# Performance work log

Measured on AMD Instinct MI355X. Metric: run time of the kernel, lower is better.

## Reference

```python
import jax, jax.numpy as jnp
import numpy as np

B, T, N, H, NHEADS, DFF, DEMO = 128, 128, 76, 64, 4, 256, 12

def _lin(x, W, b):
    # torch Linear: y = x @ W.T + b, W is [out, in]
    return jnp.matmul(x, W.T) + b

def _layernorm(x, g, b, eps=1e-7):
    mu = x.mean(-1, keepdims=True)
    var = ((x - mu) ** 2).mean(-1, keepdims=True)
    return (x - mu) / jnp.sqrt(var + eps) * g + b

def _gru_all_features(X, Wih, Whh, bih, bhh):
    # X: [B,T,N]; Wih: [N,3H] (input_size=1); Whh: [N,3H,H]; biases [N,3H]
    # PyTorch gate order: r, z, n. Returns H_seq [B,N,T,H].
    Bsz, Tlen, Nf = X.shape
    Hd = Whh.shape[-1]
    h0 = jnp.zeros((Bsz, Nf, Hd), X.dtype)
    def step(h, x_t):  # h [B,N,H], x_t [B,N]
        ih = x_t[:, :, None] * Wih[None] + bih[None]            # [B,N,3H]
        hh = jnp.einsum('bnh,ngh->bng', h, Whh) + bhh[None]     # [B,N,3H]
        r = jax.nn.sigmoid(ih[..., :Hd] + hh[..., :Hd])
        z = jax.nn.sigmoid(ih[..., Hd:2 * Hd] + hh[..., Hd:2 * Hd])
        n = jnp.tanh(ih[..., 2 * Hd:] + r * hh[..., 2 * Hd:])
        h_new = (1.0 - z) * n + z * h
        return h_new, h_new
    _, Hs = jax.lax.scan(step, h0, jnp.moveaxis(X, 1, 0))       # [T,B,N,H]
    return jnp.transpose(Hs, (1, 2, 0, 3))                      # [B,N,T,H]

def _time_attention(Hs, Wt, bt, Wx, bx, rate):
    # Hs [B,N,T,H]; Wt/Wx [N,H,H]; bt/bx [N,H]; rate [N]
    Tlen = Hs.shape[2]
    q = jnp.einsum('bnh,nkh->bnk', Hs[:, :, -1, :], Wt) + bt[None]          # [B,N,H]
    K = jnp.einsum('bnth,nkh->bntk', Hs, Wx) + bx[None, :, None, :]         # [B,N,T,H]
    dot = jnp.einsum('bnk,bntk->bnt', q, K)                                 # [B,N,T]
    tdecay = jnp.arange(1, Tlen + 1, dtype=Hs.dtype)                        # [1..T]
    ds = jax.nn.sigmoid(dot)
    denom = jax.nn.sigmoid(rate)[None, :, None] * jnp.log(2.72 + (1.0 - ds)) * tdecay
    denom = jnp.maximum(denom, 1e-6)
    e = jax.nn.relu(ds / denom)
    alpha = jax.nn.softmax(e, axis=-1)
    return jnp.einsum('bnt,bnth->bnh', alpha, Hs)                           # [B,N,H]

def _mha_decov(x, Wq, bq, Wk, bk, Wv, bv, Wo, bo, n_heads):
    Bsz, L, Dm = x.shape
    dk = Dm // n_heads
    def split(t):
        return t.reshape(Bsz, L, n_heads, dk).transpose(0, 2, 1, 3)
    q, k, v = split(_lin(x, Wq, bq)), split(_lin(x, Wk, bk)), split(_lin(x, Wv, bv))
    scores = jnp.matmul(q, k.transpose(0, 1, 3, 2)) / (dk ** 0.5)
    attn = jax.nn.softmax(scores, axis=-1)
    head = jnp.matmul(attn, v)                                              # [B,h,L,dk]
    merged = head.transpose(0, 2, 1, 3).reshape(Bsz, L, Dm)
    out = _lin(merged, Wo, bo)
    U = merged.reshape(Bsz * L, Dm)
    U = U - U.mean(0, keepdims=True)
    C = (U.T @ U) / max(Bsz * L, 1)
    decov = 0.5 * ((C ** 2).sum() - (jnp.diag(C) ** 2).sum())
    return out, decov

def setup_inputs():
    key = jax.random.key(0)
    ks = jax.random.split(key, 32)
    s = 0.08
    def rn(k, shape):
        return jax.random.normal(k, shape, jnp.float32) * s
    inp = {
        'X': jax.random.normal(ks[0], (B, T, N), jnp.float32),
        'D': jax.random.normal(ks[1], (B, DEMO), jnp.float32),
        'gru_Wih': rn(ks[2], (N, 3 * H)),
        'gru_Whh': rn(ks[3], (N, 3 * H, H)),
        'gru_bih': jnp.zeros((N, 3 * H), jnp.float32),
        'gru_bhh': jnp.zeros((N, 3 * H), jnp.float32),
        'att_Wt': rn(ks[4], (N, H, H)),
        'att_bt': jnp.zeros((N, H), jnp.float32),
        'att_Wx': rn(ks[5], (N, H, H)),
        'att_bx': jnp.zeros((N, H), jnp.float32),
        'att_rate': jnp.zeros((N,), jnp.float32),
        'demo_W': rn(ks[6], (H, DEMO)),
        'demo_b': jnp.zeros((H,), jnp.float32),
        'mh_Wq': rn(ks[7], (H, H)), 'mh_bq': rn(ks[8], (H,)),
        'mh_Wk': rn(ks[9], (H, H)), 'mh_bk': rn(ks[10], (H,)),
        'mh_Wv': rn(ks[11], (H, H)), 'mh_bv': rn(ks[12], (H,)),
        'mh_Wo': rn(ks[13], (H, H)), 'mh_bo': rn(ks[14], (H,)),
        'ln1_g': jnp.ones((H,), jnp.float32), 'ln1_b': jnp.zeros((H,), jnp.float32),
        'ffn_W1': rn(ks[15], (DFF, H)), 'ffn_b1': rn(ks[16], (DFF,)),
        'ffn_W2': rn(ks[17], (H, DFF)), 'ffn_b2': rn(ks[18], (H,)),
        'ln2_g': jnp.ones((H,), jnp.float32), 'ln2_b': jnp.zeros((H,), jnp.float32),
        'fa_Wq': rn(ks[19], (H, H)), 'fa_bq': rn(ks[20], (H,)),
        'fa_Wk': rn(ks[21], (H, H)), 'fa_bk': rn(ks[22], (H,)),
        'fa_Wv': rn(ks[23], (H, H)), 'fa_bv': rn(ks[24], (H,)),
        'fa_Wout': rn(ks[25], (1, H)), 'fa_bout': rn(ks[26], (1,)),
        'out0_W': rn(ks[27], (H, H)), 'out0_b': jnp.zeros((H,), jnp.float32),
        'out1_W': rn(ks[28], (1, H)), 'out1_b': jnp.zeros((1,), jnp.float32),
    }
    return inp

def _forward(X, D, gru_Wih, gru_Whh, gru_bih, gru_bhh, att_Wt, att_bt, att_Wx, att_bx,
             att_rate, demo_W, demo_b, mh_Wq, mh_bq, mh_Wk, mh_bk, mh_Wv, mh_bv, mh_Wo,
             mh_bo, ln1_g, ln1_b, ffn_W1, ffn_b1, ffn_W2, ffn_b2, ln2_g, ln2_b,
             fa_Wq, fa_bq, fa_Wk, fa_bk, fa_Wv, fa_bv, fa_Wout, fa_bout,
             out0_W, out0_b, out1_W, out1_b):
    Hs = _gru_all_features(X, gru_Wih, gru_Whh, gru_bih, gru_bhh)   # [B,N,T,H]
    F_dyn = _time_attention(Hs, att_Wt, att_bt, att_Wx, att_bx, att_rate)  # [B,N,H]
    f_demo = jnp.tanh(_lin(D, demo_W, demo_b))[:, None, :]
    F_in = jnp.concatenate([F_dyn, f_demo], axis=1)                 # [B,N+1,H]
    _, decov = _mha_decov(F_in, mh_Wq, mh_bq, mh_Wk, mh_bk, mh_Wv, mh_bv, mh_Wo, mh_bo, NHEADS)
    attn_out, _ = _mha_decov(_layernorm(F_in, ln1_g, ln1_b), mh_Wq, mh_bq, mh_Wk, mh_bk,
                             mh_Wv, mh_bv, mh_Wo, mh_bo, NHEADS)
    Y = F_in + attn_out
    z = _layernorm(Y, ln2_g, ln2_b)
    Z = Y + _lin(jax.nn.relu(_lin(z, ffn_W1, ffn_b1)), ffn_W2, ffn_b2)
    # FinalAttentionQKV
    Q = _lin(Z, fa_Wq, fa_bq)
    K = _lin(Z, fa_Wk, fa_bk)
    V = _lin(Z, fa_Wv, fa_bv)
    scores = _lin(Q * K, fa_Wout, fa_bout)[..., 0]                  # [B,L]
    alpha = jax.nn.softmax(scores, axis=1)
    s = jnp.einsum('bl,blh->bh', alpha, V)
    h = jax.nn.relu(_lin(s, out0_W, out0_b))
    y_prob = jax.nn.sigmoid(_lin(h, out1_W, out1_b))
    return y_prob, decov

def reference(X, D, gru_Wih, gru_Whh, gru_bih, gru_bhh, att_Wt, att_bt, att_Wx, att_bx,
              att_rate, demo_W, demo_b, mh_Wq, mh_bq, mh_Wk, mh_bk, mh_Wv, mh_bv, mh_Wo,
              mh_bo, ln1_g, ln1_b, ffn_W1, ffn_b1, ffn_W2, ffn_b2, ln2_g, ln2_b,
              fa_Wq, fa_bq, fa_Wk, fa_bk, fa_Wv, fa_bv, fa_Wout, fa_bout,
              out0_W, out0_b, out1_W, out1_b):
    return _forward(X, D, gru_Wih, gru_Whh, gru_bih, gru_bhh, att_Wt, att_bt, att_Wx,
                    att_bx, att_rate, demo_W, demo_b, mh_Wq, mh_bq, mh_Wk, mh_bk, mh_Wv,
                    mh_bv, mh_Wo, mh_bo, ln1_g, ln1_b, ffn_W1, ffn_b1, ffn_W2, ffn_b2,
                    ln2_g, ln2_b, fa_Wq, fa_bq, fa_Wk, fa_bk, fa_Wv, fa_bv, fa_Wout,
                    fa_bout, out0_W, out0_b, out1_W, out1_b)
```

## Files before the change

kernel.cpp:

```cpp
#include <hip/hip_runtime.h>
#include <math.h>

#define B_ 128
#define T_ 128
#define NF 76
#define HD 64
#define LQ 77

typedef __attribute__((ext_vector_type(8))) short short8v;
typedef __attribute__((ext_vector_type(4))) short short4v;
typedef __attribute__((ext_vector_type(4))) float f32x4;

__device__ __forceinline__ float frcp(float x) { return __builtin_amdgcn_rcpf(x); }
__device__ __forceinline__ float sigmf(float x) { return frcp(1.0f + __expf(-x)); }
__device__ __forceinline__ float sigm2(float x) { return frcp(1.0f + __builtin_amdgcn_exp2f(-x)); }
__device__ __forceinline__ float tanh_fast(float x) { return 2.0f * frcp(1.0f + __expf(-2.0f * x)) - 1.0f; }
__device__ __forceinline__ short tobf(float x) {
    unsigned u = __float_as_uint(x);
    u += 0x7FFF + ((u >> 16) & 1);
    return (short)(u >> 16);
}
__device__ __forceinline__ float bflo(unsigned u) { return __uint_as_float(u << 16); }
__device__ __forceinline__ float bfhi(unsigned u) { return __uint_as_float(u & 0xffff0000u); }

__global__ __launch_bounds__(256) void k_gru0(
    const float* __restrict__ X, const float* __restrict__ Wih,
    const float* __restrict__ Whh, const float* __restrict__ bih,
    const float* __restrict__ bhh,
    const float* __restrict__ Wt, const float* __restrict__ bt,
    const float* __restrict__ Wx, const float* __restrict__ bx,
    short* __restrict__ Hsg, float* __restrict__ qxg, float* __restrict__ qbg)
{
    __shared__ short As[8][16 * 68];
    __shared__ float xs[16 * 129];
    __shared__ float q1[16 * 65];
    __shared__ float q2[16 * 65];

    const int nf = blockIdx.y;
    const int chunk = blockIdx.x;
    const int cbase = chunk * 16;
    const int tid = threadIdx.x;
    const int w = tid >> 6;
    const int lane = tid & 63;
    const int col = lane & 15;
    const int quad = lane >> 4;

    const float S1 = 1.44269504f;
    const float S2 = 2.88539008f;

    for (int i = tid; i < 16 * T_; i += 256) {
        int b = i >> 7, t = i & 127;
        xs[b * 129 + t] = X[((size_t)(cbase + b) * T_ + t) * NF + nf];
    }

    short8v bfr[3][2];
    const float* wbase = Whh + (size_t)nf * 12288;
#pragma unroll
    for (int g3 = 0; g3 < 3; ++g3) {
        const float sc = (g3 == 2) ? S2 : S1;
#pragma unroll
        for (int k2 = 0; k2 < 2; ++k2) {
            int g = 64 * g3 + 16 * w + col;
            const float* src = wbase + g * 64 + 32 * k2 + quad * 8;
            float4 f0 = *(const float4*)src;
            float4 f1 = *(const float4*)(src + 4);
            short8v fr;
            fr[0] = tobf(f0.x * sc); fr[1] = tobf(f0.y * sc);
            fr[2] = tobf(f0.z * sc); fr[3] = tobf(f0.w * sc);
            fr[4] = tobf(f1.x * sc); fr[5] = tobf(f1.y * sc);
            fr[6] = tobf(f1.z * sc); fr[7] = tobf(f1.w * sc);
            bfr[g3][k2] = fr;
        }
    }

    const int c = 16 * w + col;
    const int base = nf * 192;
    const float wr = Wih[base + c] * S1;
    const float wz = Wih[base + 64 + c] * S1;
    const float wn = Wih[base + 128 + c] * S2;
    const float br = (bih[base + c] + bhh[base + c]) * S1;
    const float bz = (bih[base + 64 + c] + bhh[base + 64 + c]) * S1;
    const float bnn = bih[base + 128 + c] * S2;
    const float bhn = bhh[base + 128 + c] * S2;

    for (int i = tid; i < 16 * 68; i += 256) As[7][i] = 0;
    float hold[4];
#pragma unroll
    for (int r = 0; r < 4; ++r) hold[r] = 0.0f;
    __syncthreads();

    for (int t = 0; t < T_; ++t) {
        const int rb = (t + 7) & 7;
        const int wb = t & 7;
        const short* ap = &As[rb][col * 68 + quad * 8];
        short4v a0 = *(const short4v*)ap;
        short4v a1 = *(const short4v*)(ap + 4);
        short4v a2 = *(const short4v*)(ap + 32);
        short4v a3 = *(const short4v*)(ap + 36);
        short8v A0 = {a0[0], a0[1], a0[2], a0[3], a1[0], a1[1], a1[2], a1[3]};
        short8v A1 = {a2[0], a2[1], a2[2], a2[3], a3[0], a3[1], a3[2], a3[3]};

        f32x4 acc[3];
#pragma unroll
        for (int g3 = 0; g3 < 3; ++g3) {
            f32x4 a = {0.0f, 0.0f, 0.0f, 0.0f};
            a = __builtin_amdgcn_mfma_f32_16x16x32_bf16(A0, bfr[g3][0], a, 0, 0, 0);
            a = __builtin_amdgcn_mfma_f32_16x16x32_bf16(A1, bfr[g3][1], a, 0, 0, 0);
            acc[g3] = a;
        }

#pragma unroll
        for (int r = 0; r < 4; ++r) {
            float xv = xs[(quad * 4 + r) * 129 + t];
            float rr = sigm2(xv * wr + br + acc[0][r]);
            float zz = sigm2(xv * wz + bz + acc[1][r]);
            float nn = 2.0f * sigm2(xv * wn + bnn + rr * (acc[2][r] + bhn)) - 1.0f;
            hold[r] = nn + zz * (hold[r] - nn);
        }

#pragma unroll
        for (int r = 0; r < 4; ++r)
            As[wb][(quad * 4 + r) * 68 + c] = tobf(hold[r]);
        __syncthreads();

        if ((t & 7) == 7) {
            const int oct = tid & 7, bb = (tid >> 3) & 15, k0 = tid >> 7;
            short4v r0[4], r1[4];
#pragma unroll
            for (int s = 0; s < 4; ++s) {
                const short* p = &As[k0 + 2 * s][bb * 68 + oct * 8];
                r0[s] = *(const short4v*)p;
                r1[s] = *(const short4v*)(p + 4);
            }
            __syncthreads();
            const size_t gbase =
                (((size_t)nf * 128 + cbase + bb) * 128 + (t - 7)) * 64 + oct * 8;
#pragma unroll
            for (int s = 0; s < 4; ++s) {
                short8v v = {r0[s][0], r0[s][1], r0[s][2], r0[s][3],
                             r1[s][0], r1[s][1], r1[s][2], r1[s][3]};
                *(short8v*)(Hsg + gbase + (size_t)(k0 + 2 * s) * 64) = v;
            }
        }
    }

#pragma unroll
    for (int r = 0; r < 4; ++r)
        q1[(quad * 4 + r) * 65 + c] = hold[r];
    __syncthreads();
    for (int o = tid; o < 16 * 64; o += 256) {
        int b = o >> 6, k = o & 63;
        const float* wrow = Wt + ((size_t)nf * 64 + k) * 64;
        float a = bt[nf * 64 + k];
#pragma unroll 8
        for (int h = 0; h < 64; h += 4) {
            float4 wv = *(const float4*)&wrow[h];
            a += q1[b * 65 + h] * wv.x + q1[b * 65 + h + 1] * wv.y
               + q1[b * 65 + h + 2] * wv.z + q1[b * 65 + h + 3] * wv.w;
        }
        q2[b * 65 + k] = a;
    }
    __syncthreads();
    for (int o = tid; o < 16 * 64; o += 256) {
        int b = o >> 6, h = o & 63;
        float a = 0.0f;
#pragma unroll 8
        for (int k = 0; k < 64; ++k)
            a += q2[b * 65 + k] * Wx[((size_t)nf * 64 + k) * 64 + h];
        qxg[((size_t)nf * 128 + cbase + b) * 64 + h] = a;
    }
    for (int b = tid; b < 16; b += 256) {
        float a = 0.0f;
        for (int k = 0; k < 64; ++k) a += q2[b * 65 + k] * bx[nf * 64 + k];
        qbg[nf * 128 + cbase + b] = a;
    }
}

__global__ __launch_bounds__(128) void k_att(
    const short* __restrict__ Hsg, const float* __restrict__ qxg,
    const float* __restrict__ qbg, const float* __restrict__ rate,
    const float* __restrict__ D, const float* __restrict__ dW,
    const float* __restrict__ db, float* __restrict__ Sz,
    float* __restrict__ Fin)
{
    const int nf = blockIdx.x, b = blockIdx.y;
    const int tid = threadIdx.x;

    if (nf == NF) {
        if (tid < 64) {
            float acc = db[tid];
            for (int j = 0; j < 12; ++j) acc += D[b * 12 + j] * dW[tid * 12 + j];
            Fin[((size_t)b * LQ + 76) * HD + tid] = tanh_fast(acc);
        }
        int s0 = b * 33;
        for (int k = tid; k < 33; k += 128) {
            int idx = s0 + k;
            if (idx < 4161) Sz[idx] = 0.0f;
        }
        return;
    }

    __shared__ float wsum[128 * 69];
    __shared__ float wl[128];
    __shared__ float qxl[64];
    __shared__ float pn[2][68];
    __shared__ float pd[2];
    if (tid < 64) qxl[tid] = qxg[((size_t)nf * 128 + b) * 64 + tid];
    const float qb = qbg[nf * 128 + b];
    const float sigr = sigmf(rate[nf]);

    uint4 rv[8];
    const uint4* src = (const uint4*)(Hsg + (((size_t)nf * 128 + b) * 128 + tid) * 64);
#pragma unroll
    for (int k = 0; k < 8; ++k) rv[k] = src[k];
    __syncthreads();

    float a = qb;
#pragma unroll
    for (int k = 0; k < 8; ++k) {
        a += bflo(rv[k].x) * qxl[k * 8 + 0] + bfhi(rv[k].x) * qxl[k * 8 + 1]
           + bflo(rv[k].y) * qxl[k * 8 + 2] + bfhi(rv[k].y) * qxl[k * 8 + 3]
           + bflo(rv[k].z) * qxl[k * 8 + 4] + bfhi(rv[k].z) * qxl[k * 8 + 5]
           + bflo(rv[k].w) * qxl[k * 8 + 6] + bfhi(rv[k].w) * qxl[k * 8 + 7];
    }
    float ds = sigmf(a);
    float dn = fmaxf(sigr * __logf(2.72f + (1.0f - ds)) * (float)(tid + 1), 1e-6f);
    float e = fmaxf(ds * frcp(dn), 0.0f);
    float w = __expf(e);
    wl[tid] = w;
#pragma unroll
    for (int k = 0; k < 8; ++k) {
        float* d = &wsum[tid * 69 + k * 8];
        d[0] = w * bflo(rv[k].x); d[1] = w * bfhi(rv[k].x);
        d[2] = w * bflo(rv[k].y); d[3] = w * bfhi(rv[k].y);
        d[4] = w * bflo(rv[k].z); d[5] = w * bfhi(rv[k].z);
        d[6] = w * bflo(rv[k].w); d[7] = w * bfhi(rv[k].w);
    }
    __syncthreads();
    {
        int ch = tid & 63, half = tid >> 6;
        float acc = 0.0f, den = 0.0f;
        int t0 = half * 64;
        for (int t = t0; t < t0 + 64; ++t) {
            acc += wsum[t * 69 + ch];
            den += wl[t];
        }
        pn[half][ch] = acc;
        if (ch == 0) pd[half] = den;
    }
    __syncthreads();
    if (tid < 64) {
        float num = pn[0][tid] + pn[1][tid];
        float den = pd[0] + pd[1];
        Fin[((size_t)b * LQ + nf) * HD + tid] = num * frcp(den);
    }
}

// ... 529 lines not shown
                int b = o >> 6, h = o & 63;
                float a = 0.0f;
#pragma unroll 8
                for (int k = 0; k < 64; ++k)
                    a += q2[b * 65 + k] * Wx[((size_t)nf * 64 + k) * 64 + h];
                q1[b * 65 + h] = a;
            }
            for (int b = tid; b < 16; b += 128) {
                float a = 0.0f;
                for (int k = 0; k < 64; ++k) a += q2[b * 65 + k] * bx[nf * 64 + k];
                qbs[b] = a;
            }
            __syncthreads();
#pragma unroll
            for (int r = 0; r < 4; ++r) {
                qbv[r] = qbs[quad * 4 + r];
#pragma unroll
                for (int s = 0; s < 2; ++s)
                    qxv[s][r] = q1[(quad * 4 + r) * 65 + 32 * w + 16 * s + col];
                den[r] = 0.0f; num[0][r] = 0.0f; num[1][r] = 0.0f;
            }
            __syncthreads();
        }
    }
#pragma unroll
    for (int s = 0; s < 2; ++s)
#pragma unroll
        for (int r = 0; r < 4; ++r) {
            int b = cbase + quad * 4 + r;
            int c = 32 * w + 16 * s + col;
            Fin[((size_t)b * LQ + nf) * HD + c] = num[s][r] * frcp(den[r]);
        }
}

extern "C" void kernel_launch(void* const* d_in, const int* in_sizes, int n_in,
                              void* d_out, int out_size, void* d_ws, size_t ws_size,
                              hipStream_t stream)
{
    (void)in_sizes; (void)n_in; (void)out_size;
    const float* X     = (const float*)d_in[0];
    const float* D     = (const float*)d_in[1];
    const float* gWih  = (const float*)d_in[2];
    const float* gWhh  = (const float*)d_in[3];
    const float* gbih  = (const float*)d_in[4];
    const float* gbhh  = (const float*)d_in[5];
    const float* aWt   = (const float*)d_in[6];
    const float* abt   = (const float*)d_in[7];
    const float* aWx   = (const float*)d_in[8];
    const float* abx   = (const float*)d_in[9];
    const float* arate = (const float*)d_in[10];
    const float* dW    = (const float*)d_in[11];
    const float* db    = (const float*)d_in[12];
    const float* mWq   = (const float*)d_in[13]; const float* mbq = (const float*)d_in[14];
    const float* mWk   = (const float*)d_in[15]; const float* mbk = (const float*)d_in[16];
    const float* mWv   = (const float*)d_in[17]; const float* mbv = (const float*)d_in[18];
    const float* mWo   = (const float*)d_in[19]; const float* mbo = (const float*)d_in[20];
    const float* l1g   = (const float*)d_in[21]; const float* l1b = (const float*)d_in[22];
    const float* fW1   = (const float*)d_in[23]; const float* fb1 = (const float*)d_in[24];
    const float* fW2   = (const float*)d_in[25]; const float* fb2 = (const float*)d_in[26];
    const float* l2g   = (const float*)d_in[27]; const float* l2b = (const float*)d_in[28];
    const float* faWq  = (const float*)d_in[29]; const float* fabq = (const float*)d_in[30];
    const float* faWk  = (const float*)d_in[31]; const float* fabk = (const float*)d_in[32];
    const float* faWv  = (const float*)d_in[33]; const float* fabv = (const float*)d_in[34];
    const float* faWo  = (const float*)d_in[35]; const float* fabo = (const float*)d_in[36];
    const float* o0W   = (const float*)d_in[37]; const float* o0b  = (const float*)d_in[38];
    const float* o1W   = (const float*)d_in[39]; const float* o1b  = (const float*)d_in[40];

    float* ws  = (float*)d_ws;
    float* Fin = ws;
    float* M1  = Fin + 630784;
    float* M2  = M1  + 630784;
    float* S   = M2  + 630784;
    float* MU  = S   + 4096;
    unsigned* cnt = (unsigned*)(MU + 64);
    float* qxg = MU + 128;
    float* scout = qxg + 622592;
    short* Hsg = (short*)(scout + 9856);
    const size_t need = (size_t)(630784 * 3 + 4096 + 128 + 622592 + 9856) * 4
                        + (size_t)79691776 * 2;
    float* outp = (float*)d_out;
    float* qbg = scout;

    if (ws_size >= need) {
        k_gru0<<<dim3(8, NF), 256, 0, stream>>>(X, gWih, gWhh, gbih, gbhh,
                                                aWt, abt, aWx, abx, Hsg, qxg, qbg);
        k_att<<<dim3(NF + 1, B_), 128, 0, stream>>>(Hsg, qxg, qbg, arate,
                                                    D, dW, db, S, Fin);
    } else {
        k_gru_mfma<<<dim3(8, NF), 128, 0, stream>>>(X, gWih, gWhh, gbih, gbhh,
                                                    aWt, abt, aWx, abx, arate, Fin);
        k_demo<<<B_, 64, 0, stream>>>(D, dW, db, Fin);
        k_zero<<<1, 256, 0, stream>>>(S);
    }
    k_mha2<<<dim3(B_, 4, 2), 256, 0, stream>>>(Fin, mWq, mbq, mWk, mbk, mWv, mbv,
                                               l1g, l1b, M1, M2);
    k_zff<<<616, 256, 0, stream>>>(Fin, M2, mWo, mbo, l2g, l2b,
                                   fW1, fb1, fW2, fb2,
                                   faWq, fabq, faWk, fabk, faWv, fabv,
                                   faWo, fabo, scout);
    k_cov<<<dim3(16, 32), 256, 0, stream>>>(M1, S, MU, cnt, outp);
    k_head<<<B_, 128, 0, stream>>>(M2, scout, o0W, o0b, o1W, o1b, outp);
}
```

Before: 519.6 us.

## Process two GRU features per block to interleave independent recurrences

Each GRU block now handles two adjacent features, so two independent recurrent chains share one time-step loop and barrier, which lets MFMA and transcendental latency of one chain overlap the other. Gate biases are folded into the MFMA accumulator init, the x loads become float2, and s_setprio is raised around the MFMA section. The grid halves to 8x38 blocks, so fewer waves are resident across the device, and register use per thread roughly doubles for the weight fragments.

```diff
diff --git a/kernel.cpp b/kernel.cpp
--- a/kernel.cpp
+++ b/kernel.cpp
@@ -31,14 +31,13 @@
     const float* __restrict__ Wx, const float* __restrict__ bx,
     short* __restrict__ Hsg, float* __restrict__ qxg, float* __restrict__ qbg)
 {
-    __shared__ short As[8][16 * 68];
-    __shared__ float xs[16 * 129];
+    __shared__ short As[2][8][16 * 68];
+    __shared__ float2 xs2[16 * 129];
     __shared__ float q1[16 * 65];
     __shared__ float q2[16 * 65];
 
-    const int nf = blockIdx.y;
-    const int chunk = blockIdx.x;
-    const int cbase = chunk * 16;
+    const int nf0 = blockIdx.y * 2;
+    const int cbase = blockIdx.x * 16;
     const int tid = threadIdx.x;
     const int w = tid >> 6;
     const int lane = tid & 63;
@@ -50,129 +49,167 @@
 
     for (int i = tid; i < 16 * T_; i += 256) {
         int b = i >> 7, t = i & 127;
-        xs[b * 129 + t] = X[((size_t)(cbase + b) * T_ + t) * NF + nf];
-    }
-
-    short8v bfr[3][2];
-    const float* wbase = Whh + (size_t)nf * 12288;
-#pragma unroll
-    for (int g3 = 0; g3 < 3; ++g3) {
-        const float sc = (g3 == 2) ? S2 : S1;
-#pragma unroll
-        for (int k2 = 0; k2 < 2; ++k2) {
-            int g = 64 * g3 + 16 * w + col;
-            const float* src = wbase + g * 64 + 32 * k2 + quad * 8;
-            float4 f0 = *(const float4*)src;
-            float4 f1 = *(const float4*)(src + 4);
-            short8v fr;
-            fr[0] = tobf(f0.x * sc); fr[1] = tobf(f0.y * sc);
-            fr[2] = tobf(f0.z * sc); fr[3] = tobf(f0.w * sc);
-            fr[4] = tobf(f1.x * sc); fr[5] = tobf(f1.y * sc);
-            fr[6] = tobf(f1.z * sc); fr[7] = tobf(f1.w * sc);
-            bfr[g3][k2] = fr;
-        }
+        xs2[b * 129 + t] = *(const float2*)&X[((size_t)(cbase + b) * T_ + t) * NF + nf0];
     }
 
     const int c = 16 * w + col;
-    const int base = nf * 192;
-    const float wr = Wih[base + c] * S1;
-    const float wz = Wih[base + 64 + c] * S1;
-    const float wn = Wih[base + 128 + c] * S2;
-    const float br = (bih[base + c] + bhh[base + c]) * S1;
-    const float bz = (bih[base + 64 + c] + bhh[base + 64 + c]) * S1;
-    const float bnn = bih[base + 128 + c] * S2;
-    const float bhn = bhh[base + 128 + c] * S2;
-
-    for (int i = tid; i < 16 * 68; i += 256) As[7][i] = 0;
-    float hold[4];
-#pragma unroll
-    for (int r = 0; r < 4; ++r) hold[r] = 0.0f;
+
+    short8v bfr[2][3][2];
+    f32x4 biasC[2][3];
+    float wrv[2], wzv[2], wnv[2], bnnv[2];
+#pragma unroll
+    for (int f = 0; f < 2; ++f) {
+        const float* wbase = Whh + (size_t)(nf0 + f) * 12288;
+#pragma unroll
+        for (int g3 = 0; g3 < 3; ++g3) {
+            const float sc = (g3 == 2) ? S2 : S1;
+#pragma unroll
+            for (int k2 = 0; k2 < 2; ++k2) {
+                int g = 64 * g3 + 16 * w + col;
+                const float* src = wbase + g * 64 + 32 * k2 + quad * 8;
+                float4 f0 = *(const float4*)src;
+                float4 f1 = *(const float4*)(src + 4);
+                short8v fr;
+                fr[0] = tobf(f0.x * sc); fr[1] = tobf(f0.y * sc);
+                fr[2] = tobf(f0.z * sc); fr[3] = tobf(f0.w * sc);
+                fr[4] = tobf(f1.x * sc); fr[5] = tobf(f1.y * sc);
+                fr[6] = tobf(f1.z * sc); fr[7] = tobf(f1.w * sc);
+                bfr[f][g3][k2] = fr;
+            }
+        }
+        const int base = (nf0 + f) * 192;
+        wrv[f] = Wih[base + c] * S1;
+        wzv[f] = Wih[base + 64 + c] * S1;
+        wnv[f] = Wih[base + 128 + c] * S2;
+        bnnv[f] = bih[base + 128 + c] * S2;
+        float brr = (bih[base + c] + bhh[base + c]) * S1;
+        float bzz = (bih[base + 64 + c] + bhh[base + 64 + c]) * S1;
+        float bhn = bhh[base + 128 + c] * S2;
+        biasC[f][0] = (f32x4){brr, brr, brr, brr};
+        biasC[f][1] = (f32x4){bzz, bzz, bzz, bzz};
+        biasC[f][2] = (f32x4){bhn, bhn, bhn, bhn};
+    }
+
+    {
+        short* Ap = &As[0][0][0];
+        for (int i = tid; i < 1088; i += 256) {
+            Ap[7 * 1088 + i] = 0;
+            Ap[15 * 1088 + i] = 0;
+        }
+    }
+    float hold[2][4];
+#pragma unroll
+    for (int f = 0; f < 2; ++f)
+#pragma unroll
+        for (int r = 0; r < 4; ++r) hold[f][r] = 0.0f;
     __syncthreads();
 
     for (int t = 0; t < T_; ++t) {
         const int rb = (t + 7) & 7;
         const int wb = t & 7;
-        const short* ap = &As[rb][col * 68 + quad * 8];
-        short4v a0 = *(const short4v*)ap;
-        short4v a1 = *(const short4v*)(ap + 4);
-        short4v a2 = *(const short4v*)(ap + 32);
-        short4v a3 = *(const short4v*)(ap + 36);
-        short8v A0 = {a0[0], a0[1], a0[2], a0[3], a1[0], a1[1], a1[2], a1[3]};
-        short8v A1 = {a2[0], a2[1], a2[2], a2[3], a3[0], a3[1], a3[2], a3[3]};
-
-        f32x4 acc[3];
-#pragma unroll
-        for (int g3 = 0; g3 < 3; ++g3) {
-            f32x4 a = {0.0f, 0.0f, 0.0f, 0.0f};
-            a = __builtin_amdgcn_mfma_f32_16x16x32_bf16(A0, bfr[g3][0], a, 0, 0, 0);
-            a = __builtin_amdgcn_mfma_f32_16x16x32_bf16(A1, bfr[g3][1], a, 0, 0, 0);
-            acc[g3] = a;
-        }
+
+        short8v A0[2], A1[2];
+#pragma unroll
+        for (int f = 0; f < 2; ++f) {
+            const short* ap = &As[f][rb][col * 68 + quad * 8];
+            short4v a0 = *(const short4v*)ap;
+            short4v a1 = *(const short4v*)(ap + 4);
+            short4v a2 = *(const short4v*)(ap + 32);
+            short4v a3 = *(const short4v*)(ap + 36);
+            A0[f] = (short8v){a0[0], a0[1], a0[2], a0[3], a1[0], a1[1], a1[2], a1[3]};
+            A1[f] = (short8v){a2[0], a2[1], a2[2], a2[3], a3[0], a3[1], a3[2], a3[3]};
+        }
+
+        __builtin_amdgcn_s_setprio(1);
+        f32x4 acc[2][3];
+#pragma unroll
+        for (int f = 0; f < 2; ++f)
+#pragma unroll
+            for (int g3 = 0; g3 < 3; ++g3) {
+                f32x4 a = __builtin_amdgcn_mfma_f32_16x16x32_bf16(
+                    A0[f], bfr[f][g3][0], biasC[f][g3], 0, 0, 0);
+                acc[f][g3] = __builtin_amdgcn_mfma_f32_16x16x32_bf16(
+                    A1[f], bfr[f][g3][1], a, 0, 0, 0);
+            }
+        __builtin_amdgcn_s_setprio(0);
 
 #pragma unroll
         for (int r = 0; r < 4; ++r) {
-            float xv = xs[(quad * 4 + r) * 129 + t];
-            float rr = sigm2(xv * wr + br + acc[0][r]);
-            float zz = sigm2(xv * wz + bz + acc[1][r]);
-            float nn = 2.0f * sigm2(xv * wn + bnn + rr * (acc[2][r] + bhn)) - 1.0f;
-            hold[r] = nn + zz * (hold[r] - nn);
-        }
-
-#pragma unroll
-        for (int r = 0; r < 4; ++r)
-            As[wb][(quad * 4 + r) * 68 + c] = tobf(hold[r]);
+            float2 xv2 = xs2[(quad * 4 + r) * 129 + t];
+            float xvf[2] = {xv2.x, xv2.y};
+#pragma unroll
+            for (int f = 0; f < 2; ++f) {
+                float xv = xvf[f];
+                float rr = sigm2(fmaf(xv, wrv[f], acc[f][0][r]));
+                float zz = sigm2(fmaf(xv, wzv[f], acc[f][1][r]));
+                float uu = sigm2(fmaf(rr, acc[f][2][r], fmaf(xv, wnv[f], bnnv[f])));
+                float nn = fmaf(2.0f, uu, -1.0f);
+                hold[f][r] = fmaf(zz, hold[f][r] - nn, nn);
+                As[f][wb][(quad * 4 + r) * 68 + c] = tobf(hold[f][r]);
+            }
+        }
         __syncthreads();
 
         if ((t & 7) == 7) {
             const int oct = tid & 7, bb = (tid >> 3) & 15, k0 = tid >> 7;
-            short4v r0[4], r1[4];
-#pragma unroll
-            for (int s = 0; s < 4; ++s) {
-                const short* p = &As[k0 + 2 * s][bb * 68 + oct * 8];
-                r0[s] = *(const short4v*)p;
-                r1[s] = *(const short4v*)(p + 4);
-            }
+            short4v r0[2][4], r1[2][4];
+#pragma unroll
+            for (int f = 0; f < 2; ++f)
+#pragma unroll
+                for (int s = 0; s < 4; ++s) {
+                    const short* p = &As[f][k0 + 2 * s][bb * 68 + oct * 8];
+                    r0[f][s] = *(const short4v*)p;
+                    r1[f][s] = *(const short4v*)(p + 4);
+                }
             __syncthreads();
-            const size_t gbase =
-                (((size_t)nf * 128 + cbase + bb) * 128 + (t - 7)) * 64 + oct * 8;
-#pragma unroll
-            for (int s = 0; s < 4; ++s) {
-                short8v v = {r0[s][0], r0[s][1], r0[s][2], r0[s][3],
-                             r1[s][0], r1[s][1], r1[s][2], r1[s][3]};
-                *(short8v*)(Hsg + gbase + (size_t)(k0 + 2 * s) * 64) = v;
-            }
-        }
-    }
-
-#pragma unroll
-    for (int r = 0; r < 4; ++r)
-        q1[(quad * 4 + r) * 65 + c] = hold[r];
-    __syncthreads();
-    for (int o = tid; o < 16 * 64; o += 256) {
-        int b = o >> 6, k = o & 63;
-        const float* wrow = Wt + ((size_t)nf * 64 + k) * 64;
-        float a = bt[nf * 64 + k];
+#pragma unroll
+            for (int f = 0; f < 2; ++f) {
+                const size_t gbase =
+                    (((size_t)(nf0 + f) * 128 + cbase + bb) * 128 + (t - 7)) * 64 + oct * 8;
+#pragma unroll
+                for (int s = 0; s < 4; ++s) {
+                    short8v v = {r0[f][s][0], r0[f][s][1], r0[f][s][2], r0[f][s][3],
+                                 r1[f][s][0], r1[f][s][1], r1[f][s][2], r1[f][s][3]};
+                    *(short8v*)(Hsg + gbase + (size_t)(k0 + 2 * s) * 64) = v;
+                }
+            }
+        }
+    }
+
+#pragma unroll
+    for (int f = 0; f < 2; ++f) {
+        const int nf = nf0 + f;
+        __syncthreads();
+#pragma unroll
+        for (int r = 0; r < 4; ++r)
+            q1[(quad * 4 + r) * 65 + c] = hold[f][r];
+        __syncthreads();
+        for (int o = tid; o < 16 * 64; o += 256) {
+            int b = o >> 6, k = o & 63;
+            const float* wrow = Wt + ((size_t)nf * 64 + k) * 64;
+            float a = bt[nf * 64 + k];
 #pragma unroll 8
-        for (int h = 0; h < 64; h += 4) {
-            float4 wv = *(const float4*)&wrow[h];
-            a += q1[b * 65 + h] * wv.x + q1[b * 65 + h + 1] * wv.y
-               + q1[b * 65 + h + 2] * wv.z + q1[b * 65 + h + 3] * wv.w;
-        }
-        q2[b * 65 + k] = a;
-    }
-    __syncthreads();
-    for (int o = tid; o < 16 * 64; o += 256) {
-        int b = o >> 6, h = o & 63;
-        float a = 0.0f;
+            for (int h = 0; h < 64; h += 4) {
+                float4 wv = *(const float4*)&wrow[h];
+                a += q1[b * 65 + h] * wv.x + q1[b * 65 + h + 1] * wv.y
+                   + q1[b * 65 + h + 2] * wv.z + q1[b * 65 + h + 3] * wv.w;
+            }
+            q2[b * 65 + k] = a;
+        }
+        __syncthreads();
+        for (int o = tid; o < 16 * 64; o += 256) {
+            int b = o >> 6, h = o & 63;
+            float a = 0.0f;
 #pragma unroll 8
-        for (int k = 0; k < 64; ++k)
-            a += q2[b * 65 + k] * Wx[((size_t)nf * 64 + k) * 64 + h];
-        qxg[((size_t)nf * 128 + cbase + b) * 64 + h] = a;
-    }
-    for (int b = tid; b < 16; b += 256) {
-        float a = 0.0f;
-        for (int k = 0; k < 64; ++k) a += q2[b * 65 + k] * bx[nf * 64 + k];
-        qbg[nf * 128 + cbase + b] = a;
+            for (int k = 0; k < 64; ++k)
+                a += q2[b * 65 + k] * Wx[((size_t)nf * 64 + k) * 64 + h];
+            qxg[((size_t)nf * 128 + cbase + b) * 64 + h] = a;
+        }
+        for (int b = tid; b < 16; b += 256) {
+            float a = 0.0f;
+            for (int k = 0; k < 64; ++k) a += q2[b * 65 + k] * bx[nf * 64 + k];
+            qbg[nf * 128 + cbase + b] = a;
+        }
     }
 }
 
@@ -868,7 +905,7 @@
     float* qbg = scout;
 
     if (ws_size >= need) {
-        k_gru0<<<dim3(8, NF), 256, 0, stream>>>(X, gWih, gWhh, gbih, gbhh,
+        k_gru0<<<dim3(8, 38), 256, 0, stream>>>(X, gWih, gWhh, gbih, gbhh,
                                                 aWt, abt, aWx, abx, Hsg, qxg, qbg);
         k_att<<<dim3(NF + 1, B_), 128, 0, stream>>>(Hsg, qxg, qbg, arate,
                                                     D, dW, db, S, Fin);
```

Measured after the change: 561.7 us. 8.1% more time.

## Run each GRU recurrence block as a single wavefront to drop barriers

Applied to the files above, without the earlier changes.

The GRU kernel moves from four wavefronts per block, each owning 16 hidden columns, to one 64-lane wavefront that owns all 64 columns. Each lane now keeps 24 weight fragments in registers and issues 24 MFMAs per step. Because the whole block is one wavefront, the per-step __syncthreads and the periodic spill barriers go away, so the sequential recurrence no longer pays for cross-wave synchronisation. The time loop is unrolled by 8 with s_setprio around the MFMAs, and the epilogue projections are restructured for a single wave. The cost is much higher register pressure and four times fewer threads across the grid to hide latency.

```diff
diff --git a/kernel.cpp b/kernel.cpp
--- a/kernel.cpp
+++ b/kernel.cpp
@@ -23,7 +23,7 @@
 __device__ __forceinline__ float bflo(unsigned u) { return __uint_as_float(u << 16); }
 __device__ __forceinline__ float bfhi(unsigned u) { return __uint_as_float(u & 0xffff0000u); }
 
-__global__ __launch_bounds__(256) void k_gru0(
+__global__ __launch_bounds__(64) void k_gru0(
     const float* __restrict__ X, const float* __restrict__ Wih,
     const float* __restrict__ Whh, const float* __restrict__ bih,
     const float* __restrict__ bhh,
@@ -31,148 +31,185 @@
     const float* __restrict__ Wx, const float* __restrict__ bx,
     short* __restrict__ Hsg, float* __restrict__ qxg, float* __restrict__ qbg)
 {
-    __shared__ short As[8][16 * 68];
-    __shared__ float xs[16 * 129];
-    __shared__ float q1[16 * 65];
-    __shared__ float q2[16 * 65];
+    __shared__ short As[8 * 1088];
+    __shared__ float scratch[2176];
 
     const int nf = blockIdx.y;
-    const int chunk = blockIdx.x;
-    const int cbase = chunk * 16;
-    const int tid = threadIdx.x;
-    const int w = tid >> 6;
-    const int lane = tid & 63;
-    const int col = lane & 15;
-    const int quad = lane >> 4;
+    const int cbase = blockIdx.x * 16;
+    const int lane = threadIdx.x;
+    const int c15 = lane & 15;
+    const int q = lane >> 4;
 
     const float S1 = 1.44269504f;
     const float S2 = 2.88539008f;
 
-    for (int i = tid; i < 16 * T_; i += 256) {
+    for (int i = lane; i < 2048; i += 64) {
         int b = i >> 7, t = i & 127;
-        xs[b * 129 + t] = X[((size_t)(cbase + b) * T_ + t) * NF + nf];
-    }
-
-    short8v bfr[3][2];
+        scratch[b * 130 + t] = X[((size_t)(cbase + b) * T_ + t) * NF + nf];
+    }
+
+    short8v bfr[3][4][2];
     const float* wbase = Whh + (size_t)nf * 12288;
 #pragma unroll
     for (int g3 = 0; g3 < 3; ++g3) {
         const float sc = (g3 == 2) ? S2 : S1;
 #pragma unroll
-        for (int k2 = 0; k2 < 2; ++k2) {
-            int g = 64 * g3 + 16 * w + col;
-            const float* src = wbase + g * 64 + 32 * k2 + quad * 8;
-            float4 f0 = *(const float4*)src;
-            float4 f1 = *(const float4*)(src + 4);
-            short8v fr;
-            fr[0] = tobf(f0.x * sc); fr[1] = tobf(f0.y * sc);
-            fr[2] = tobf(f0.z * sc); fr[3] = tobf(f0.w * sc);
-            fr[4] = tobf(f1.x * sc); fr[5] = tobf(f1.y * sc);
-            fr[6] = tobf(f1.z * sc); fr[7] = tobf(f1.w * sc);
-            bfr[g3][k2] = fr;
-        }
-    }
-
-    const int c = 16 * w + col;
-    const int base = nf * 192;
-    const float wr = Wih[base + c] * S1;
-    const float wz = Wih[base + 64 + c] * S1;
-    const float wn = Wih[base + 128 + c] * S2;
-    const float br = (bih[base + c] + bhh[base + c]) * S1;
-    const float bz = (bih[base + 64 + c] + bhh[base + 64 + c]) * S1;
-    const float bnn = bih[base + 128 + c] * S2;
-    const float bhn = bhh[base + 128 + c] * S2;
-
-    for (int i = tid; i < 16 * 68; i += 256) As[7][i] = 0;
-    float hold[4];
-#pragma unroll
-    for (int r = 0; r < 4; ++r) hold[r] = 0.0f;
-    __syncthreads();
-
-    for (int t = 0; t < T_; ++t) {
-        const int rb = (t + 7) & 7;
-        const int wb = t & 7;
-        const short* ap = &As[rb][col * 68 + quad * 8];
-        short4v a0 = *(const short4v*)ap;
-        short4v a1 = *(const short4v*)(ap + 4);
-        short4v a2 = *(const short4v*)(ap + 32);
-        short4v a3 = *(const short4v*)(ap + 36);
-        short8v A0 = {a0[0], a0[1], a0[2], a0[3], a1[0], a1[1], a1[2], a1[3]};
-        short8v A1 = {a2[0], a2[1], a2[2], a2[3], a3[0], a3[1], a3[2], a3[3]};
-
-        f32x4 acc[3];
-#pragma unroll
-        for (int g3 = 0; g3 < 3; ++g3) {
-            f32x4 a = {0.0f, 0.0f, 0.0f, 0.0f};
-            a = __builtin_amdgcn_mfma_f32_16x16x32_bf16(A0, bfr[g3][0], a, 0, 0, 0);
-            a = __builtin_amdgcn_mfma_f32_16x16x32_bf16(A1, bfr[g3][1], a, 0, 0, 0);
-            acc[g3] = a;
-        }
-
-#pragma unroll
-        for (int r = 0; r < 4; ++r) {
-            float xv = xs[(quad * 4 + r) * 129 + t];
-            float rr = sigm2(xv * wr + br + acc[0][r]);
-            float zz = sigm2(xv * wz + bz + acc[1][r]);
-            float nn = 2.0f * sigm2(xv * wn + bnn + rr * (acc[2][r] + bhn)) - 1.0f;
-            hold[r] = nn + zz * (hold[r] - nn);
-        }
-
+        for (int n = 0; n < 4; ++n)
+#pragma unroll
+            for (int k2 = 0; k2 < 2; ++k2) {
+                int g = 64 * g3 + 16 * n + c15;
+                const float* src = wbase + g * 64 + 32 * k2 + q * 8;
+                float4 f0 = *(const float4*)src;
+                float4 f1 = *(const float4*)(src + 4);
+                short8v fr;
+                fr[0] = tobf(f0.x * sc); fr[1] = tobf(f0.y * sc);
+                fr[2] = tobf(f0.z * sc); fr[3] = tobf(f0.w * sc);
+                fr[4] = tobf(f1.x * sc); fr[5] = tobf(f1.y * sc);
+                fr[6] = tobf(f1.z * sc); fr[7] = tobf(f1.w * sc);
+                bfr[g3][n][k2] = fr;
+            }
+    }
+
+    float wrv[4], wzv[4], wnv[4], brv[4], bzv[4], bnnv[4], bhnv[4];
+    {
+        const int base = nf * 192;
+#pragma unroll
+        for (int n = 0; n < 4; ++n) {
+            int j = 16 * n + c15;
+            wrv[n] = Wih[base + j] * S1;
+            brv[n] = (bih[base + j] + bhh[base + j]) * S1;
+            wzv[n] = Wih[base + 64 + j] * S1;
+            bzv[n] = (bih[base + 64 + j] + bhh[base + 64 + j]) * S1;
+            wnv[n] = Wih[base + 128 + j] * S2;
+            bnnv[n] = bih[base + 128 + j] * S2;
+            bhnv[n] = bhh[base + 128 + j] * S2;
+        }
+    }
+
+    {
+        short8v z8 = {0, 0, 0, 0, 0, 0, 0, 0};
+        for (int i = lane; i < 136; i += 64)
+            *(short8v*)&As[7 * 1088 + i * 8] = z8;
+    }
+    float hold[4][4];
+#pragma unroll
+    for (int n = 0; n < 4; ++n)
+#pragma unroll
+        for (int r = 0; r < 4; ++r) hold[n][r] = 0.0f;
+
+    const f32x4 zc = {0.0f, 0.0f, 0.0f, 0.0f};
+
+    for (int tt = 0; tt < 16; ++tt) {
+#pragma unroll
+        for (int u = 0; u < 8; ++u) {
+            const int t = tt * 8 + u;
+            const int rb = (u + 7) & 7;
+            const int wb = u;
+            const short* ap = &As[rb * 1088 + c15 * 68 + q * 8];
+            short4v a0 = *(const short4v*)ap;
+            short4v a1 = *(const short4v*)(ap + 4);
+            short4v a2 = *(const short4v*)(ap + 32);
+            short4v a3 = *(const short4v*)(ap + 36);
+            short8v A0 = {a0[0], a0[1], a0[2], a0[3], a1[0], a1[1], a1[2], a1[3]};
+            short8v A1 = {a2[0], a2[1], a2[2], a2[3], a3[0], a3[1], a3[2], a3[3]};
+
+            float xv[4];
+#pragma unroll
+            for (int r = 0; r < 4; ++r)
+                xv[r] = scratch[(q * 4 + r) * 130 + t];
+
+            __builtin_amdgcn_s_setprio(1);
+            f32x4 acc[3][4];
+#pragma unroll
+            for (int g3 = 0; g3 < 3; ++g3)
+#pragma unroll
+                for (int n = 0; n < 4; ++n) {
+                    f32x4 a = __builtin_amdgcn_mfma_f32_16x16x32_bf16(
+                        A0, bfr[g3][n][0], zc, 0, 0, 0);
+                    acc[g3][n] = __builtin_amdgcn_mfma_f32_16x16x32_bf16(
+                        A1, bfr[g3][n][1], a, 0, 0, 0);
+                }
+            __builtin_amdgcn_s_setprio(0);
+
+#pragma unroll
+            for (int n = 0; n < 4; ++n)
+#pragma unroll
+                for (int r = 0; r < 4; ++r) {
+                    float rr = sigm2(fmaf(xv[r], wrv[n], brv[n]) + acc[0][n][r]);
+                    float zz = sigm2(fmaf(xv[r], wzv[n], bzv[n]) + acc[1][n][r]);
+                    float uu = sigm2(fmaf(rr, acc[2][n][r] + bhnv[n],
+                                          fmaf(xv[r], wnv[n], bnnv[n])));
+                    float nn = fmaf(2.0f, uu, -1.0f);
+                    hold[n][r] = fmaf(zz, hold[n][r] - nn, nn);
+                    As[wb * 1088 + (q * 4 + r) * 68 + 16 * n + c15] = tobf(hold[n][r]);
+                }
+        }
+        {
+            const int oct = lane & 7, b8 = lane >> 3;
+#pragma unroll
+            for (int s = 0; s < 16; ++s) {
+                int k = s >> 1, b = b8 + 8 * (s & 1);
+                const short* p = &As[k * 1088 + b * 68 + oct * 8];
+                uint2 lo = *(const uint2*)p;
+                uint2 hi = *(const uint2*)(p + 4);
+                uint4 v = {lo.x, lo.y, hi.x, hi.y};
+                *(uint4*)(Hsg + (((size_t)nf * 128 + cbase + b) * 128
+                                 + (tt * 8 + k)) * 64 + oct * 8) = v;
+            }
+        }
+    }
+
+    float* h32 = scratch;
+    float* q2s = scratch + 1088;
+#pragma unroll
+    for (int n = 0; n < 4; ++n)
 #pragma unroll
         for (int r = 0; r < 4; ++r)
-            As[wb][(quad * 4 + r) * 68 + c] = tobf(hold[r]);
-        __syncthreads();
-
-        if ((t & 7) == 7) {
-            const int oct = tid & 7, bb = (tid >> 3) & 15, k0 = tid >> 7;
-            short4v r0[4], r1[4];
-#pragma unroll
-            for (int s = 0; s < 4; ++s) {
-                const short* p = &As[k0 + 2 * s][bb * 68 + oct * 8];
-                r0[s] = *(const short4v*)p;
-                r1[s] = *(const short4v*)(p + 4);
-            }
-            __syncthreads();
-            const size_t gbase =
-                (((size_t)nf * 128 + cbase + bb) * 128 + (t - 7)) * 64 + oct * 8;
-#pragma unroll
-            for (int s = 0; s < 4; ++s) {
-                short8v v = {r0[s][0], r0[s][1], r0[s][2], r0[s][3],
-                             r1[s][0], r1[s][1], r1[s][2], r1[s][3]};
-                *(short8v*)(Hsg + gbase + (size_t)(k0 + 2 * s) * 64) = v;
-            }
-        }
-    }
-
-#pragma unroll
-    for (int r = 0; r < 4; ++r)
-        q1[(quad * 4 + r) * 65 + c] = hold[r];
-    __syncthreads();
-    for (int o = tid; o < 16 * 64; o += 256) {
-        int b = o >> 6, k = o & 63;
-        const float* wrow = Wt + ((size_t)nf * 64 + k) * 64;
-        float a = bt[nf * 64 + k];
-#pragma unroll 8
-        for (int h = 0; h < 64; h += 4) {
-            float4 wv = *(const float4*)&wrow[h];
-            a += q1[b * 65 + h] * wv.x + q1[b * 65 + h + 1] * wv.y
-               + q1[b * 65 + h + 2] * wv.z + q1[b * 65 + h + 3] * wv.w;
-        }
-        q2[b * 65 + k] = a;
-    }
-    __syncthreads();
-    for (int o = tid; o < 16 * 64; o += 256) {
-        int b = o >> 6, h = o & 63;
+            h32[(q * 4 + r) * 68 + 16 * n + c15] = hold[n][r];
+
+    {
+        const int b = lane & 15, kg = lane >> 4;
+#pragma unroll 4
+        for (int kk = 0; kk < 16; ++kk) {
+            int k = kg * 16 + kk;
+            const float4* wrow = (const float4*)(Wt + ((size_t)nf * 64 + k) * 64);
+            float a = bt[nf * 64 + k];
+#pragma unroll 4
+            for (int h4 = 0; h4 < 16; ++h4) {
+                float4 wv = wrow[h4];
+                float4 hh = *(const float4*)&h32[b * 68 + h4 * 4];
+                a += hh.x * wv.x + hh.y * wv.y + hh.z * wv.z + hh.w * wv.w;
+            }
+            q2s[b * 68 + k] = a;
+        }
+    }
+
+    {
+        float accq[16];
+#pragma unroll
+        for (int b = 0; b < 16; ++b) accq[b] = 0.0f;
+        const float* wxb = Wx + (size_t)nf * 4096 + lane;
+        for (int k4 = 0; k4 < 16; ++k4) {
+            float w0 = wxb[(k4 * 4 + 0) * 64];
+            float w1 = wxb[(k4 * 4 + 1) * 64];
+            float w2 = wxb[(k4 * 4 + 2) * 64];
+            float w3 = wxb[(k4 * 4 + 3) * 64];
+#pragma unroll
+            for (int b = 0; b < 16; ++b) {
+                float4 qv = *(const float4*)&q2s[b * 68 + k4 * 4];
+                accq[b] += qv.x * w0 + qv.y * w1 + qv.z * w2 + qv.w * w3;
+            }
+        }
+#pragma unroll
+        for (int b = 0; b < 16; ++b)
+            qxg[((size_t)nf * 128 + cbase + b) * 64 + lane] = accq[b];
+    }
+
+    if (lane < 16) {
         float a = 0.0f;
-#pragma unroll 8
         for (int k = 0; k < 64; ++k)
-            a += q2[b * 65 + k] * Wx[((size_t)nf * 64 + k) * 64 + h];
-        qxg[((size_t)nf * 128 + cbase + b) * 64 + h] = a;
-    }
-    for (int b = tid; b < 16; b += 256) {
-        float a = 0.0f;
-        for (int k = 0; k < 64; ++k) a += q2[b * 65 + k] * bx[nf * 64 + k];
-        qbg[nf * 128 + cbase + b] = a;
+            a += q2s[lane * 68 + k] * bx[nf * 64 + k];
+        qbg[nf * 128 + cbase + lane] = a;
     }
 }
 
@@ -868,8 +905,8 @@
     float* qbg = scout;
 
     if (ws_size >= need) {
-        k_gru0<<<dim3(8, NF), 256, 0, stream>>>(X, gWih, gWhh, gbih, gbhh,
-                                                aWt, abt, aWx, abx, Hsg, qxg, qbg);
+        k_gru0<<<dim3(8, NF), 64, 0, stream>>>(X, gWih, gWhh, gbih, gbhh,
+                                               aWt, abt, aWx, abx, Hsg, qxg, qbg);
         k_att<<<dim3(NF + 1, B_), 128, 0, stream>>>(Hsg, qxg, qbg, arate,
                                                     D, dW, db, S, Fin);
     } else {
```

New measurement: 573.7 us. 1.1x slower.

## Split GRU recurrence into 8-batch blocks with 2 waves each covering two column tiles

Applied to the files above, without the earlier changes.

The GRU kernel now processes 8 batch rows per block using 128 threads (2 waves), each wave handling two 16-column tiles. The grid doubles to 16x76 blocks, which gives more parallelism for the serial time loop. The batch dimension is padded to 16 inside the MFMA, so half the rows are wasted work. Biases are folded into the MFMA accumulator init, and s_setprio is wrapped around the MFMA section. Each block keeps more weight fragments in registers, and the final projection layout is adjusted to match.

```diff
diff --git a/kernel.cpp b/kernel.cpp
--- a/kernel.cpp
+++ b/kernel.cpp
@@ -23,7 +23,7 @@
 __device__ __forceinline__ float bflo(unsigned u) { return __uint_as_float(u << 16); }
 __device__ __forceinline__ float bfhi(unsigned u) { return __uint_as_float(u & 0xffff0000u); }
 
-__global__ __launch_bounds__(256) void k_gru0(
+__global__ __launch_bounds__(128) void k_gru0(
     const float* __restrict__ X, const float* __restrict__ Wih,
     const float* __restrict__ Whh, const float* __restrict__ bih,
     const float* __restrict__ bhh,
@@ -31,68 +31,73 @@
     const float* __restrict__ Wx, const float* __restrict__ bx,
     short* __restrict__ Hsg, float* __restrict__ qxg, float* __restrict__ qbg)
 {
-    __shared__ short As[8][16 * 68];
-    __shared__ float xs[16 * 129];
-    __shared__ float q1[16 * 65];
-    __shared__ float q2[16 * 65];
+    __shared__ short As[8 * 1088];
+    __shared__ float scratch[1104];
 
     const int nf = blockIdx.y;
-    const int chunk = blockIdx.x;
-    const int cbase = chunk * 16;
+    const int cbase = blockIdx.x * 8;
     const int tid = threadIdx.x;
     const int w = tid >> 6;
     const int lane = tid & 63;
-    const int col = lane & 15;
+    const int c15 = lane & 15;
     const int quad = lane >> 4;
 
     const float S1 = 1.44269504f;
     const float S2 = 2.88539008f;
 
-    for (int i = tid; i < 16 * T_; i += 256) {
+    for (int i = tid; i < 8 * 128; i += 128) {
         int b = i >> 7, t = i & 127;
-        xs[b * 129 + t] = X[((size_t)(cbase + b) * T_ + t) * NF + nf];
-    }
-
-    short8v bfr[3][2];
+        scratch[b * 130 + t] = X[((size_t)(cbase + b) * T_ + t) * NF + nf];
+    }
+
+    short8v bfr[3][2][2];
+    f32x4 biasC[3][2];
+    float wrv[2], wzv[2], wnv[2], bnnv[2];
     const float* wbase = Whh + (size_t)nf * 12288;
-#pragma unroll
-    for (int g3 = 0; g3 < 3; ++g3) {
-        const float sc = (g3 == 2) ? S2 : S1;
-#pragma unroll
-        for (int k2 = 0; k2 < 2; ++k2) {
-            int g = 64 * g3 + 16 * w + col;
-            const float* src = wbase + g * 64 + 32 * k2 + quad * 8;
-            float4 f0 = *(const float4*)src;
-            float4 f1 = *(const float4*)(src + 4);
-            short8v fr;
-            fr[0] = tobf(f0.x * sc); fr[1] = tobf(f0.y * sc);
-            fr[2] = tobf(f0.z * sc); fr[3] = tobf(f0.w * sc);
-            fr[4] = tobf(f1.x * sc); fr[5] = tobf(f1.y * sc);
-            fr[6] = tobf(f1.z * sc); fr[7] = tobf(f1.w * sc);
-            bfr[g3][k2] = fr;
-        }
-    }
-
-    const int c = 16 * w + col;
     const int base = nf * 192;
-    const float wr = Wih[base + c] * S1;
-    const float wz = Wih[base + 64 + c] * S1;
-    const float wn = Wih[base + 128 + c] * S2;
-    const float br = (bih[base + c] + bhh[base + c]) * S1;
-    const float bz = (bih[base + 64 + c] + bhh[base + 64 + c]) * S1;
-    const float bnn = bih[base + 128 + c] * S2;
-    const float bhn = bhh[base + 128 + c] * S2;
-
-    for (int i = tid; i < 16 * 68; i += 256) As[7][i] = 0;
-    float hold[4];
-#pragma unroll
-    for (int r = 0; r < 4; ++r) hold[r] = 0.0f;
+#pragma unroll
+    for (int n2 = 0; n2 < 2; ++n2) {
+        const int j = 16 * (2 * w + n2) + c15;
+#pragma unroll
+        for (int g3 = 0; g3 < 3; ++g3) {
+            const float sc = (g3 == 2) ? S2 : S1;
+#pragma unroll
+            for (int k2 = 0; k2 < 2; ++k2) {
+                const float* src = wbase + (64 * g3 + j) * 64 + 32 * k2 + quad * 8;
+                float4 f0 = *(const float4*)src;
+                float4 f1 = *(const float4*)(src + 4);
+                short8v fr;
+                fr[0] = tobf(f0.x * sc); fr[1] = tobf(f0.y * sc);
+                fr[2] = tobf(f0.z * sc); fr[3] = tobf(f0.w * sc);
+                fr[4] = tobf(f1.x * sc); fr[5] = tobf(f1.y * sc);
+                fr[6] = tobf(f1.z * sc); fr[7] = tobf(f1.w * sc);
+                bfr[g3][n2][k2] = fr;
+            }
+        }
+        wrv[n2] = Wih[base + j] * S1;
+        wzv[n2] = Wih[base + 64 + j] * S1;
+        wnv[n2] = Wih[base + 128 + j] * S2;
+        bnnv[n2] = bih[base + 128 + j] * S2;
+        float brr = (bih[base + j] + bhh[base + j]) * S1;
+        float bzz = (bih[base + 64 + j] + bhh[base + 64 + j]) * S1;
+        float bhn = bhh[base + 128 + j] * S2;
+        biasC[0][n2] = (f32x4){brr, brr, brr, brr};
+        biasC[1][n2] = (f32x4){bzz, bzz, bzz, bzz};
+        biasC[2][n2] = (f32x4){bhn, bhn, bhn, bhn};
+    }
+
+    for (int i = tid; i < 1088; i += 128) As[7 * 1088 + i] = 0;
+    float hold[2][4];
+#pragma unroll
+    for (int n2 = 0; n2 < 2; ++n2)
+#pragma unroll
+        for (int r = 0; r < 4; ++r) hold[n2][r] = 0.0f;
     __syncthreads();
 
     for (int t = 0; t < T_; ++t) {
         const int rb = (t + 7) & 7;
         const int wb = t & 7;
-        const short* ap = &As[rb][col * 68 + quad * 8];
+        const short* ap = &As[rb * 1088 + c15 * 68 + quad * 8];
         short4v a0 = *(const short4v*)ap;
         short4v a1 = *(const short4v*)(ap + 4);
         short4v a2 = *(const short4v*)(ap + 32);
@@ -100,41 +105,51 @@
         short8v A0 = {a0[0], a0[1], a0[2], a0[3], a1[0], a1[1], a1[2], a1[3]};
         short8v A1 = {a2[0], a2[1], a2[2], a2[3], a3[0], a3[1], a3[2], a3[3]};
 
-        f32x4 acc[3];
-#pragma unroll
-        for (int g3 = 0; g3 < 3; ++g3) {
-            f32x4 a = {0.0f, 0.0f, 0.0f, 0.0f};
-            a = __builtin_amdgcn_mfma_f32_16x16x32_bf16(A0, bfr[g3][0], a, 0, 0, 0);
-            a = __builtin_amdgcn_mfma_f32_16x16x32_bf16(A1, bfr[g3][1], a, 0, 0, 0);
-            acc[g3] = a;
-        }
-
-#pragma unroll
-        for (int r = 0; r < 4; ++r) {
-            float xv = xs[(quad * 4 + r) * 129 + t];
-            float rr = sigm2(xv * wr + br + acc[0][r]);
-            float zz = sigm2(xv * wz + bz + acc[1][r]);
-            float nn = 2.0f * sigm2(xv * wn + bnn + rr * (acc[2][r] + bhn)) - 1.0f;
-            hold[r] = nn + zz * (hold[r] - nn);
-        }
-
+        float xv[4];
 #pragma unroll
         for (int r = 0; r < 4; ++r)
-            As[wb][(quad * 4 + r) * 68 + c] = tobf(hold[r]);
+            xv[r] = scratch[((quad * 4 + r) & 7) * 130 + t];
+
+        __builtin_amdgcn_s_setprio(1);
+        f32x4 acc[3][2];
+#pragma unroll
+        for (int g3 = 0; g3 < 3; ++g3)
+#pragma unroll
+            for (int n2 = 0; n2 < 2; ++n2) {
+                f32x4 a = __builtin_amdgcn_mfma_f32_16x16x32_bf16(
+                    A0, bfr[g3][n2][0], biasC[g3][n2], 0, 0, 0);
+                acc[g3][n2] = __builtin_amdgcn_mfma_f32_16x16x32_bf16(
+                    A1, bfr[g3][n2][1], a, 0, 0, 0);
+            }
+        __builtin_amdgcn_s_setprio(0);
+
+#pragma unroll
+        for (int n2 = 0; n2 < 2; ++n2)
+#pragma unroll
+            for (int r = 0; r < 4; ++r) {
+                float rr = sigm2(fmaf(xv[r], wrv[n2], acc[0][n2][r]));
+                float zz = sigm2(fmaf(xv[r], wzv[n2], acc[1][n2][r]));
+                float uu = sigm2(fmaf(rr, acc[2][n2][r],
+                                      fmaf(xv[r], wnv[n2], bnnv[n2])));
+                float nn = fmaf(2.0f, uu, -1.0f);
+                hold[n2][r] = fmaf(zz, hold[n2][r] - nn, nn);
+                As[wb * 1088 + (quad * 4 + r) * 68 + 16 * (2 * w + n2) + c15]
+                    = tobf(hold[n2][r]);
+            }
         __syncthreads();
 
         if ((t & 7) == 7) {
-            const int oct = tid & 7, bb = (tid >> 3) & 15, k0 = tid >> 7;
+            const int oct = tid & 7, row = (tid >> 3) & 7, k0 = tid >> 6;
             short4v r0[4], r1[4];
 #pragma unroll
             for (int s = 0; s < 4; ++s) {
-                const short* p = &As[k0 + 2 * s][bb * 68 + oct * 8];
+                const short* p = &As[(k0 + 2 * s) * 1088 + row * 68 + oct * 8];
                 r0[s] = *(const short4v*)p;
                 r1[s] = *(const short4v*)(p + 4);
             }
             __syncthreads();
             const size_t gbase =
-                (((size_t)nf * 128 + cbase + bb) * 128 + (t - 7)) * 64 + oct * 8;
+                (((size_t)nf * 128 + cbase + row) * 128 + (t - 7)) * 64 + oct * 8;
 #pragma unroll
             for (int s = 0; s < 4; ++s) {
                 short8v v = {r0[s][0], r0[s][1], r0[s][2], r0[s][3],
@@ -144,35 +159,44 @@
         }
     }
 
-#pragma unroll
-    for (int r = 0; r < 4; ++r)
-        q1[(quad * 4 + r) * 65 + c] = hold[r];
-    __syncthreads();
-    for (int o = tid; o < 16 * 64; o += 256) {
+    __syncthreads();
+    float* h32 = scratch;
+    float* q2s = scratch + 544;
+    if (quad < 2) {
+#pragma unroll
+        for (int n2 = 0; n2 < 2; ++n2)
+#pragma unroll
+            for (int r = 0; r < 4; ++r)
+                h32[(quad * 4 + r) * 68 + 16 * (2 * w + n2) + c15] = hold[n2][r];
+    }
+    __syncthreads();
+
+    for (int o = tid; o < 512; o += 128) {
         int b = o >> 6, k = o & 63;
-        const float* wrow = Wt + ((size_t)nf * 64 + k) * 64;
+        const float4* wrow = (const float4*)(Wt + ((size_t)nf * 64 + k) * 64);
         float a = bt[nf * 64 + k];
-#pragma unroll 8
-        for (int h = 0; h < 64; h += 4) {
-            float4 wv = *(const float4*)&wrow[h];
-            a += q1[b * 65 + h] * wv.x + q1[b * 65 + h + 1] * wv.y
-               + q1[b * 65 + h + 2] * wv.z + q1[b * 65 + h + 3] * wv.w;
-        }
-        q2[b * 65 + k] = a;
-    }
-    __syncthreads();
-    for (int o = tid; o < 16 * 64; o += 256) {
-        int b = o >> 6, h = o & 63;
+#pragma unroll 4
+        for (int h4 = 0; h4 < 16; ++h4) {
+            float4 wv = wrow[h4];
+            float4 hh = *(const float4*)&h32[b * 68 + h4 * 4];
+            a += hh.x * wv.x + hh.y * wv.y + hh.z * wv.z + hh.w * wv.w;
+        }
+        q2s[b * 68 + k] = a;
+    }
+    __syncthreads();
+    for (int o = tid; o < 512; o += 128) {
+        int b = o >> 6, hh = o & 63;
         float a = 0.0f;
 #pragma unroll 8
         for (int k = 0; k < 64; ++k)
-            a += q2[b * 65 + k] * Wx[((size_t)nf * 64 + k) * 64 + h];
-        qxg[((size_t)nf * 128 + cbase + b) * 64 + h] = a;
-    }
-    for (int b = tid; b < 16; b += 256) {
+            a += q2s[b * 68 + k] * Wx[((size_t)nf * 64 + k) * 64 + hh];
+        qxg[((size_t)nf * 128 + cbase + b) * 64 + hh] = a;
+    }
+    if (tid < 8) {
         float a = 0.0f;
-        for (int k = 0; k < 64; ++k) a += q2[b * 65 + k] * bx[nf * 64 + k];
-        qbg[nf * 128 + cbase + b] = a;
+        for (int k = 0; k < 64; ++k)
+            a += q2s[tid * 68 + k] * bx[nf * 64 + k];
+        qbg[nf * 128 + cbase + tid] = a;
     }
 }
 
@@ -868,8 +892,8 @@
     float* qbg = scout;
 
     if (ws_size >= need) {
-        k_gru0<<<dim3(8, NF), 256, 0, stream>>>(X, gWih, gWhh, gbih, gbhh,
-                                                aWt, abt, aWx, abx, Hsg, qxg, qbg);
+        k_gru0<<<dim3(16, NF), 128, 0, stream>>>(X, gWih, gWhh, gbih, gbhh,
+                                                 aWt, abt, aWx, abx, Hsg, qxg, qbg);
         k_att<<<dim3(NF + 1, B_), 128, 0, stream>>>(Hsg, qxg, qbg, arate,
                                                     D, dW, db, S, Fin);
     } else {
```

Measured after the change: 602.8 us. 16.0% more time.
